# Optimization experiments

Measured on AMD Instinct MI355X. Metric: run time of the kernel, lower is better.

Reference implementation:

```python
import jax, jax.numpy as jnp
import numpy as np
from jax import lax

B, L, H = 32, 4096, 512  # batch, v_len (encoder frames), hidden_dim


def setup_inputs() -> dict:
    key = jax.random.key(0)
    ks = jax.random.split(key, 9)
    return {
        "query": jax.random.normal(ks[0], (B, 1, H), dtype=jnp.float32),
        "value": jax.random.normal(ks[1], (B, L, H), dtype=jnp.float32),
        "last_attn": jax.random.uniform(ks[2], (B, L), dtype=jnp.float32),
        # conv1d: in_channels=1, out_channels=H, kernel_size=3
        "conv_w": jax.random.normal(ks[3], (H, 1, 3), dtype=jnp.float32) * 0.1,
        "conv_b": jax.random.normal(ks[4], (H,), dtype=jnp.float32) * 0.1,
        "Wq": jax.random.normal(ks[5], (H, H), dtype=jnp.float32) / np.sqrt(H),
        "Wv": jax.random.normal(ks[6], (H, H), dtype=jnp.float32) / np.sqrt(H),
        "Ws": jax.random.normal(ks[7], (H,), dtype=jnp.float32) / np.sqrt(H),  # score_proj weight (1,H) flattened
        "bs": jnp.zeros((), dtype=jnp.float32),  # score_proj bias
        "bias": jax.random.uniform(ks[8], (H,), minval=-0.1, maxval=0.1, dtype=jnp.float32),
    }


def reference(query, value, last_attn, conv_w, conv_b, Wq, Wv, Ws, bs, bias):
    # conv1d over previous alignment: (B,1,L) -> (B,H,L), then transpose to (B,L,H)
    conv_attn = lax.conv_general_dilated(
        last_attn[:, None, :], conv_w, window_strides=(1,), padding=[(1, 1)],
        dimension_numbers=("NCH", "OIH", "NCH"))
    conv_attn = conv_attn.transpose(0, 2, 1) + conv_b[None, None, :]  # (B,L,H)

    q = jnp.einsum("bqh,oh->bqo", query, Wq)   # (B,1,H), broadcasts over L
    v = jnp.einsum("blh,oh->blo", value, Wv)   # (B,L,H)
    e = jnp.tanh(q + v + conv_attn + bias)     # (B,L,H)
    score = jnp.einsum("blh,h->bl", e, Ws) + bs  # (B,L)

    # smoothing=True branch: sigmoid + sum-normalize
    score = jax.nn.sigmoid(score)
    attn = score / jnp.sum(score, axis=-1, keepdims=True)  # (B,L)

    context = jnp.einsum("bl,blh->bh", attn, value)  # (B,H)
    out = jnp.concatenate([context, query[:, 0, :]], axis=1)  # (B,2H)
    return out, attn
```

## Files before the change

### kernel.cpp

```cpp
#include <hip/hip_runtime.h>
#include <hip/hip_bf16.h>
#include <math.h>

#define BB 32
#define LL 4096
#define HH 512
#define TM 32

typedef __attribute__((ext_vector_type(8))) short short8;
typedef __attribute__((ext_vector_type(8))) unsigned short u16x8;
typedef __attribute__((ext_vector_type(4))) float f32x4;

__device__ __forceinline__ unsigned short f2bf(float f) {
  __hip_bfloat16 h = __float2bfloat16(f);
  unsigned short u;
  __builtin_memcpy(&u, &h, 2);
  return u;
}
__device__ __forceinline__ float bf2f(unsigned short u) {
  unsigned int x = ((unsigned int)u) << 16;
  float f;
  __builtin_memcpy(&f, &x, 4);
  return f;
}
__device__ __forceinline__ float fast_tanh(float x) {
  float e = __expf(2.f * x);
  return 1.f - 2.f / (e + 1.f);
}

__global__ __launch_bounds__(256) void prep_kernel(
    const float* __restrict__ query, const float* __restrict__ Wq,
    const float* __restrict__ bias, const float* __restrict__ conv_b,
    const float* __restrict__ Wv, float* __restrict__ base,
    unsigned short* __restrict__ wvf, float* __restrict__ ctx) {
  const int bid = blockIdx.x;
  if (bid < 64) {
    const int b = bid >> 1;
    const int o = ((bid & 1) << 8) + threadIdx.x;
    __shared__ float qrow[HH];
    for (int i = threadIdx.x; i < HH; i += 256) qrow[i] = query[b * HH + i];
    __syncthreads();
    const float* wq = Wq + (size_t)o * HH;
    float acc = 0.f;
    for (int h = 0; h < HH; h += 4) {
      float4 w = *(const float4*)(wq + h);
      acc += w.x * qrow[h] + w.y * qrow[h + 1] + w.z * qrow[h + 2] + w.w * qrow[h + 3];
    }
    base[b * HH + o] = acc + bias[o] + conv_b[o];
    ctx[b * HH + o] = 0.f;
  } else {
    const int chunk = (bid - 64) * 256 + threadIdx.x;
    const int l = chunk & 63;
    const int kk = (chunk >> 6) & 15;
    const int nb = chunk >> 10;
    const int row = nb * 16 + (l & 15);
    const int colf = kk * 32 + (l >> 4) * 8;
    const float* src = Wv + (size_t)row * HH + colf;
    u16x8 v;
    #pragma unroll
    for (int j = 0; j < 8; ++j) v[j] = f2bf(src[j]);
    *(u16x8*)(wvf + (size_t)chunk * 8) = v;
  }
}

__global__ __launch_bounds__(512, 6) void main_kernel(
    const float* __restrict__ value, const float* __restrict__ last_attn,
    const float* __restrict__ conv_w, const unsigned short* __restrict__ wvf,
    const float* __restrict__ Ws, const float* __restrict__ bs,
    const float* __restrict__ base, float* __restrict__ ctx,
    float* __restrict__ attn) {
  const int b = blockIdx.y;
  const int l0 = blockIdx.x * TM;
  const int tid = threadIdx.x;
  const int w = tid >> 6;
  const int lane = tid & 63;
  const int g = lane >> 4;
  const int r16 = lane & 15;

  __shared__ __align__(16) unsigned short A[TM * HH];
  __shared__ float la_s[TM + 2];
  __shared__ float scorered[8][TM];
  __shared__ float srow[TM];
  __shared__ float ctxsum[HH];

  char* Ab = (char*)A;

  const float* vsrc = value + (size_t)(b * LL + l0) * HH;
  #pragma unroll
  for (int i = 0; i < 4; ++i) {
    const int c = tid + i * 512;
    const int row = c >> 6;
    const int cb = c & 63;
    const float4* s4 = (const float4*)(vsrc + (size_t)row * HH + cb * 8);
    float4 lo = s4[0], hi = s4[1];
    u16x8 v;
    v[0] = f2bf(lo.x); v[1] = f2bf(lo.y); v[2] = f2bf(lo.z); v[3] = f2bf(lo.w);
    v[4] = f2bf(hi.x); v[5] = f2bf(hi.y); v[6] = f2bf(hi.z); v[7] = f2bf(hi.w);
    const int off = row * 1024 + ((cb * 16) ^ ((row & 7) << 4));
    *(u16x8*)(Ab + off) = v;
  }
  ctxsum[tid] = 0.f;
  if (tid < TM + 2) {
    int l = l0 - 1 + tid;
    la_s[tid] = (l >= 0 && l < LL) ? last_attn[b * LL + l] : 0.f;
  }
  __syncthreads();

  f32x4 acc[2][4] = {};
  const int kk0 = (blockIdx.x + (blockIdx.y << 2)) & 15;
  #pragma unroll 2
  for (int i = 0; i < 16; ++i) {
    const int kk = (kk0 + i) & 15;
    const int co = kk * 64 + g * 16;
    const int row0 = r16, row1 = 16 + r16;
    short8 a0 = *(const short8*)(Ab + row0 * 1024 + (co ^ ((row0 & 7) << 4)));
    short8 a1 = *(const short8*)(Ab + row1 * 1024 + (co ^ ((row1 & 7) << 4)));
    #pragma unroll
    for (int n = 0; n < 4; ++n) {
      short8 bf = *(const short8*)(wvf + ((size_t)((w * 4 + n) * 16 + kk) * 64 + lane) * 8);
      acc[0][n] = __builtin_amdgcn_mfma_f32_16x16x32_bf16(a0, bf, acc[0][n], 0, 0, 0);
      acc[1][n] = __builtin_amdgcn_mfma_f32_16x16x32_bf16(a1, bf, acc[1][n], 0, 0, 0);
    }
  }

  float basev[4], wsv[4], cw0[4], cw1[4], cw2[4];
  #pragma unroll
  for (int n = 0; n < 4; ++n) {
    const int col = w * 64 + n * 16 + r16;
    basev[n] = base[b * HH + col];
    wsv[n] = Ws[col];
    cw0[n] = conv_w[col * 3 + 0];
    cw1[n] = conv_w[col * 3 + 1];
    cw2[n] = conv_w[col * 3 + 2];
  }
  #pragma unroll
  for (int m = 0; m < 2; ++m) {
    #pragma unroll
    for (int j = 0; j < 4; ++j) {
      const int row = m * 16 + g * 4 + j;
      const float lam = la_s[row], laz = la_s[row + 1], lap = la_s[row + 2];
      float sum = 0.f;
      #pragma unroll
      for (int n = 0; n < 4; ++n) {
        float e = acc[m][n][j] + basev[n] + cw0[n] * lam + cw1[n] * laz + cw2[n] * lap;
        sum += fast_tanh(e) * wsv[n];
      }
      sum += __shfl_xor(sum, 1, 64);
      sum += __shfl_xor(sum, 2, 64);
      sum += __shfl_xor(sum, 4, 64);
      sum += __shfl_xor(sum, 8, 64);
      if (r16 == 0) scorered[w][row] = sum;
    }
  }
  __syncthreads();
  if (tid < TM) {
    float sc = bs[0];
    #pragma unroll
    for (int ww = 0; ww < 8; ++ww) sc += scorered[ww][tid];
    float s = 1.f / (1.f + __expf(-sc));
    srow[tid] = s;
    attn[b * LL + l0 + tid] = s;
  }
  __syncthreads();

  {
    float cs[8];
    #pragma unroll
    for (int k = 0; k < 8; ++k) cs[k] = 0.f;
    #pragma unroll
    for (int i = 0; i < 4; ++i) {
      const int row = w * 4 + i;
      const int off = row * 1024 + ((lane * 16) ^ ((row & 7) << 4));
      u16x8 v = *(const u16x8*)(Ab + off);
      const float s = srow[row];
      #pragma unroll
      for (int k = 0; k < 8; ++k) cs[k] += s * bf2f(v[k]);
    }
    #pragma unroll
    for (int k = 0; k < 8; ++k) atomicAdd(&ctxsum[lane * 8 + k], cs[k]);
  }
  __syncthreads();
  atomicAdd(&ctx[b * HH + tid], ctxsum[tid]);
}

__global__ __launch_bounds__(512) void finalize_kernel(
    const float* __restrict__ query, const float* __restrict__ ctx,
    float* __restrict__ out, float* __restrict__ attn) {
  const int b = blockIdx.x;
  const int tid = threadIdx.x;
  __shared__ float red[8];
  float s = 0.f;
  for (int l = tid; l < LL; l += 512) s += attn[b * LL + l];
  #pragma unroll
  for (int off = 32; off > 0; off >>= 1) s += __shfl_xor(s, off, 64);
  if ((tid & 63) == 0) red[tid >> 6] = s;
  __syncthreads();
  float S = 0.f;
  #pragma unroll
  for (int i = 0; i < 8; ++i) S += red[i];
  const float inv = 1.f / S;
  out[b * 2 * HH + tid] = ctx[b * HH + tid] * inv;
  out[b * 2 * HH + HH + tid] = query[b * HH + tid];
  for (int l = tid; l < LL; l += 512) attn[b * LL + l] *= inv;
}

extern "C" void kernel_launch(void* const* d_in, const int* in_sizes, int n_in,
                              void* d_out, int out_size, void* d_ws, size_t ws_size,
                              hipStream_t stream) {
  const float* query     = (const float*)d_in[0];
  const float* value     = (const float*)d_in[1];
  const float* last_attn = (const float*)d_in[2];
  const float* conv_w    = (const float*)d_in[3];
  const float* conv_b    = (const float*)d_in[4];
  const float* Wq        = (const float*)d_in[5];
  const float* Wv        = (const float*)d_in[6];
  const float* Ws        = (const float*)d_in[7];
  const float* bs        = (const float*)d_in[8];
  const float* bias      = (const float*)d_in[9];

  float* out  = (float*)d_out;
  float* attn = out + BB * 2 * HH;
  float* base = (float*)d_ws;
  float* ctx  = base + BB * HH;
  unsigned short* wvf = (unsigned short*)(ctx + BB * HH);

  prep_kernel<<<192, 256, 0, stream>>>(query, Wq, bias, conv_b, Wv, base, wvf, ctx);
  dim3 grid(LL / TM, BB);
  main_kernel<<<grid, 512, 0, stream>>>(value, last_attn, conv_w, wvf, Ws, bs,
                                        base, ctx, attn);
  finalize_kernel<<<BB, 512, 0, stream>>>(query, ctx, out, attn);
}
```

Baseline: 220.8 us.

## Spread context atomics over 8 partial buffers and fully unroll MFMA loop

Context accumulation now goes to 8 partial buffers selected by block x index, and the finalize kernel sums them, which reduces contention on global atomics. The K loop is fully unrolled with B fragments hoisted ahead of the MFMAs. The staggered k start is dropped. Score reduction now uses shared-memory atomics, which removes one barrier, and each wave recomputes the sigmoid itself. The change also adds a manual bf16 rounding, a memset launch, and lowers the occupancy hint from 6 to 4.

```diff
diff --git a/kernel.cpp b/kernel.cpp
--- a/kernel.cpp
+++ b/kernel.cpp
@@ -12,10 +12,10 @@
 typedef __attribute__((ext_vector_type(4))) float f32x4;
 
 __device__ __forceinline__ unsigned short f2bf(float f) {
-  __hip_bfloat16 h = __float2bfloat16(f);
-  unsigned short u;
-  __builtin_memcpy(&u, &h, 2);
-  return u;
+  unsigned int x;
+  __builtin_memcpy(&x, &f, 4);
+  x += 0x7fffu + ((x >> 16) & 1u);
+  return (unsigned short)(x >> 16);
 }
 __device__ __forceinline__ float bf2f(unsigned short u) {
   unsigned int x = ((unsigned int)u) << 16;
@@ -32,7 +32,7 @@
     const float* __restrict__ query, const float* __restrict__ Wq,
     const float* __restrict__ bias, const float* __restrict__ conv_b,
     const float* __restrict__ Wv, float* __restrict__ base,
-    unsigned short* __restrict__ wvf, float* __restrict__ ctx) {
+    unsigned short* __restrict__ wvf) {
   const int bid = blockIdx.x;
   if (bid < 64) {
     const int b = bid >> 1;
@@ -47,7 +47,6 @@
       acc += w.x * qrow[h] + w.y * qrow[h + 1] + w.z * qrow[h + 2] + w.w * qrow[h + 3];
     }
     base[b * HH + o] = acc + bias[o] + conv_b[o];
-    ctx[b * HH + o] = 0.f;
   } else {
     const int chunk = (bid - 64) * 256 + threadIdx.x;
     const int l = chunk & 63;
@@ -63,14 +62,15 @@
   }
 }
 
-__global__ __launch_bounds__(512, 6) void main_kernel(
+__global__ __launch_bounds__(512, 4) void main_kernel(
     const float* __restrict__ value, const float* __restrict__ last_attn,
     const float* __restrict__ conv_w, const unsigned short* __restrict__ wvf,
     const float* __restrict__ Ws, const float* __restrict__ bs,
-    const float* __restrict__ base, float* __restrict__ ctx,
+    const float* __restrict__ base, float* __restrict__ ctxp,
     float* __restrict__ attn) {
   const int b = blockIdx.y;
-  const int l0 = blockIdx.x * TM;
+  const int gx = blockIdx.x;
+  const int l0 = gx * TM;
   const int tid = threadIdx.x;
   const int w = tid >> 6;
   const int lane = tid & 63;
@@ -79,8 +79,7 @@
 
   __shared__ __align__(16) unsigned short A[TM * HH];
   __shared__ float la_s[TM + 2];
-  __shared__ float scorered[8][TM];
-  __shared__ float srow[TM];
+  __shared__ float sacc[TM];
   __shared__ float ctxsum[HH];
 
   char* Ab = (char*)A;
@@ -100,6 +99,7 @@
     *(u16x8*)(Ab + off) = v;
   }
   ctxsum[tid] = 0.f;
+  if (tid < TM) sacc[tid] = bs[0];
   if (tid < TM + 2) {
     int l = l0 - 1 + tid;
     la_s[tid] = (l >= 0 && l < LL) ? last_attn[b * LL + l] : 0.f;
@@ -107,31 +107,36 @@
   __syncthreads();
 
   f32x4 acc[2][4] = {};
-  const int kk0 = (blockIdx.x + (blockIdx.y << 2)) & 15;
-  #pragma unroll 2
-  for (int i = 0; i < 16; ++i) {
-    const int kk = (kk0 + i) & 15;
+  const short8* bp = (const short8*)wvf + (size_t)(w * 4) * 16 * 64;
+  #pragma unroll
+  for (int kk = 0; kk < 16; ++kk) {
+    short8 bf0 = bp[(0 * 16 + kk) * 64 + lane];
+    short8 bf1 = bp[(1 * 16 + kk) * 64 + lane];
+    short8 bf2 = bp[(2 * 16 + kk) * 64 + lane];
+    short8 bf3 = bp[(3 * 16 + kk) * 64 + lane];
     const int co = kk * 64 + g * 16;
-    const int row0 = r16, row1 = 16 + r16;
-    short8 a0 = *(const short8*)(Ab + row0 * 1024 + (co ^ ((row0 & 7) << 4)));
+    const int row1 = 16 + r16;
+    short8 a0 = *(const short8*)(Ab + r16  * 1024 + (co ^ ((r16  & 7) << 4)));
     short8 a1 = *(const short8*)(Ab + row1 * 1024 + (co ^ ((row1 & 7) << 4)));
-    #pragma unroll
-    for (int n = 0; n < 4; ++n) {
-      short8 bf = *(const short8*)(wvf + ((size_t)((w * 4 + n) * 16 + kk) * 64 + lane) * 8);
-      acc[0][n] = __builtin_amdgcn_mfma_f32_16x16x32_bf16(a0, bf, acc[0][n], 0, 0, 0);
-      acc[1][n] = __builtin_amdgcn_mfma_f32_16x16x32_bf16(a1, bf, acc[1][n], 0, 0, 0);
-    }
-  }
-
-  float basev[4], wsv[4], cw0[4], cw1[4], cw2[4];
+    acc[0][0] = __builtin_amdgcn_mfma_f32_16x16x32_bf16(a0, bf0, acc[0][0], 0, 0, 0);
+    acc[1][0] = __builtin_amdgcn_mfma_f32_16x16x32_bf16(a1, bf0, acc[1][0], 0, 0, 0);
+    acc[0][1] = __builtin_amdgcn_mfma_f32_16x16x32_bf16(a0, bf1, acc[0][1], 0, 0, 0);
+    acc[1][1] = __builtin_amdgcn_mfma_f32_16x16x32_bf16(a1, bf1, acc[1][1], 0, 0, 0);
+    acc[0][2] = __builtin_amdgcn_mfma_f32_16x16x32_bf16(a0, bf2, acc[0][2], 0, 0, 0);
+    acc[1][2] = __builtin_amdgcn_mfma_f32_16x16x32_bf16(a1, bf2, acc[1][2], 0, 0, 0);
+    acc[0][3] = __builtin_amdgcn_mfma_f32_16x16x32_bf16(a0, bf3, acc[0][3], 0, 0, 0);
+    acc[1][3] = __builtin_amdgcn_mfma_f32_16x16x32_bf16(a1, bf3, acc[1][3], 0, 0, 0);
+  }
+
+  float basev[4], wsv[4], cw0v[4], cw1v[4], cw2v[4];
   #pragma unroll
   for (int n = 0; n < 4; ++n) {
     const int col = w * 64 + n * 16 + r16;
     basev[n] = base[b * HH + col];
-    wsv[n] = Ws[col];
-    cw0[n] = conv_w[col * 3 + 0];
-    cw1[n] = conv_w[col * 3 + 1];
-    cw2[n] = conv_w[col * 3 + 2];
+    wsv[n]  = Ws[col];
+    cw0v[n] = conv_w[col * 3 + 0];
+    cw1v[n] = conv_w[col * 3 + 1];
+    cw2v[n] = conv_w[col * 3 + 2];
   }
   #pragma unroll
   for (int m = 0; m < 2; ++m) {
@@ -142,49 +147,42 @@
       float sum = 0.f;
       #pragma unroll
       for (int n = 0; n < 4; ++n) {
-        float e = acc[m][n][j] + basev[n] + cw0[n] * lam + cw1[n] * laz + cw2[n] * lap;
+        float e = acc[m][n][j] + basev[n] + cw0v[n] * lam + cw1v[n] * laz + cw2v[n] * lap;
         sum += fast_tanh(e) * wsv[n];
       }
       sum += __shfl_xor(sum, 1, 64);
       sum += __shfl_xor(sum, 2, 64);
       sum += __shfl_xor(sum, 4, 64);
       sum += __shfl_xor(sum, 8, 64);
-      if (r16 == 0) scorered[w][row] = sum;
+      if (r16 == 0) atomicAdd(&sacc[row], sum);
     }
   }
   __syncthreads();
-  if (tid < TM) {
-    float sc = bs[0];
-    #pragma unroll
-    for (int ww = 0; ww < 8; ++ww) sc += scorered[ww][tid];
-    float s = 1.f / (1.f + __expf(-sc));
-    srow[tid] = s;
-    attn[b * LL + l0 + tid] = s;
-  }
-  __syncthreads();
+
+  if (tid < TM) attn[b * LL + l0 + tid] = 1.f / (1.f + __expf(-sacc[tid]));
 
   {
-    float cs[8];
-    #pragma unroll
-    for (int k = 0; k < 8; ++k) cs[k] = 0.f;
+    float cacc[8];
+    #pragma unroll
+    for (int k = 0; k < 8; ++k) cacc[k] = 0.f;
     #pragma unroll
     for (int i = 0; i < 4; ++i) {
       const int row = w * 4 + i;
+      const float s = 1.f / (1.f + __expf(-sacc[row]));
       const int off = row * 1024 + ((lane * 16) ^ ((row & 7) << 4));
       u16x8 v = *(const u16x8*)(Ab + off);
-      const float s = srow[row];
       #pragma unroll
-      for (int k = 0; k < 8; ++k) cs[k] += s * bf2f(v[k]);
+      for (int k = 0; k < 8; ++k) cacc[k] += s * bf2f(v[k]);
     }
     #pragma unroll
-    for (int k = 0; k < 8; ++k) atomicAdd(&ctxsum[lane * 8 + k], cs[k]);
-  }
-  __syncthreads();
-  atomicAdd(&ctx[b * HH + tid], ctxsum[tid]);
+    for (int k = 0; k < 8; ++k) atomicAdd(&ctxsum[lane * 8 + k], cacc[k]);
+  }
+  __syncthreads();
+  atomicAdd(&ctxp[((size_t)(gx & 7) * BB + b) * HH + tid], ctxsum[tid]);
 }
 
 __global__ __launch_bounds__(512) void finalize_kernel(
-    const float* __restrict__ query, const float* __restrict__ ctx,
+    const float* __restrict__ query, const float* __restrict__ ctxp,
     float* __restrict__ out, float* __restrict__ attn) {
   const int b = blockIdx.x;
   const int tid = threadIdx.x;
@@ -199,7 +197,10 @@
   #pragma unroll
   for (int i = 0; i < 8; ++i) S += red[i];
   const float inv = 1.f / S;
-  out[b * 2 * HH + tid] = ctx[b * HH + tid] * inv;
+  float c = 0.f;
+  #pragma unroll
+  for (int k = 0; k < 8; ++k) c += ctxp[((size_t)k * BB + b) * HH + tid];
+  out[b * 2 * HH + tid] = c * inv;
   out[b * 2 * HH + HH + tid] = query[b * HH + tid];
   for (int l = tid; l < LL; l += 512) attn[b * LL + l] *= inv;
 }
@@ -221,12 +222,13 @@
   float* out  = (float*)d_out;
   float* attn = out + BB * 2 * HH;
   float* base = (float*)d_ws;
-  float* ctx  = base + BB * HH;
-  unsigned short* wvf = (unsigned short*)(ctx + BB * HH);
-
-  prep_kernel<<<192, 256, 0, stream>>>(query, Wq, bias, conv_b, Wv, base, wvf, ctx);
+  unsigned short* wvf = (unsigned short*)(base + BB * HH);
+  float* ctxp = (float*)(wvf + HH * HH);
+
+  hipMemsetAsync(ctxp, 0, 8 * BB * HH * sizeof(float), stream);
+  prep_kernel<<<192, 256, 0, stream>>>(query, Wq, bias, conv_b, Wv, base, wvf);
   dim3 grid(LL / TM, BB);
   main_kernel<<<grid, 512, 0, stream>>>(value, last_attn, conv_w, wvf, Ws, bs,
-                                        base, ctx, attn);
-  finalize_kernel<<<BB, 512, 0, stream>>>(query, ctx, out, attn);
-}
+                                        base, ctxp, attn);
+  finalize_kernel<<<BB, 512, 0, stream>>>(query, ctxp, out, attn);
+}
```

New measurement: 239.0 us. 8.2% more time.
